# Performance work log

Measured on AMD Instinct MI355X. Metric: run time of the kernel, lower is better.

The kernel has to match this reference:

```python
import jax, jax.numpy as jnp
import numpy as np

N, E, D, H, C, G, L = 100000, 1600000, 128, 4, 32, 4096, 3  # nodes, edges, h_dim, heads, head_dim, graphs, conv blocks


def setup_inputs() -> dict:
    key = jax.random.key(0)
    ks = jax.random.split(key, 24)
    s = 0.05
    w = lambda k, shape: jax.random.normal(k, shape, jnp.float32) * s
    inp = {
        "x": jax.random.normal(ks[0], (N, D), jnp.float32),
        "edge_index": jax.random.randint(ks[1], (2, E), 0, N),
        "batch": jnp.sort(jax.random.randint(ks[2], (N,), 0, G)),
        # input TransformerConv (in=D, out=C per head, H heads, beta=True)
        "in_Wq": w(ks[3], (D, D)), "in_bq": jnp.zeros((D,), jnp.float32),
        "in_Wk": w(ks[4], (D, D)), "in_bk": jnp.zeros((D,), jnp.float32),
        "in_Wv": w(ks[5], (D, D)), "in_bv": jnp.zeros((D,), jnp.float32),
        "in_Ws": w(ks[6], (D, D)), "in_bs": jnp.zeros((D,), jnp.float32),
        "in_Wbeta": w(ks[7], (3 * D,)),
        # stacked conv blocks (L of them, in=out=D)
        "blk_Wq": w(ks[8], (L, D, D)), "blk_bq": jnp.zeros((L, D), jnp.float32),
        "blk_Wk": w(ks[9], (L, D, D)), "blk_bk": jnp.zeros((L, D), jnp.float32),
        "blk_Wv": w(ks[10], (L, D, D)), "blk_bv": jnp.zeros((L, D), jnp.float32),
        "blk_Ws": w(ks[11], (L, D, D)), "blk_bs": jnp.zeros((L, D), jnp.float32),
        "blk_Wbeta": w(ks[12], (L, 3 * D)),
        # MLP head
        "W1": w(ks[13], (D, 64)), "b1": jnp.zeros((64,), jnp.float32),
        "W2": w(ks[14], (64, 32)), "b2": jnp.zeros((32,), jnp.float32),
        "W3": w(ks[15], (32, 1)), "b3": jnp.zeros((1,), jnp.float32),
    }
    return inp


def transformer_conv(x, src, dst, Wq, bq, Wk, bk, Wv, bv, Ws, bs, Wbeta):
    # PyG TransformerConv, concat=True, root_weight=True, beta=True, eval mode
    q = (x @ Wq + bq).reshape(N, H, C)
    k = (x @ Wk + bk).reshape(N, H, C)
    v = (x @ Wv + bv).reshape(N, H, C)
    # per-edge attention logits: message j=src -> i=dst
    alpha = jnp.einsum("ehc,ehc->eh", q[dst], k[src]) / jnp.sqrt(jnp.float32(C))  # [E,H]
    m = jax.ops.segment_max(alpha, dst, num_segments=N)
    m = jnp.where(jnp.isfinite(m), m, 0.0)
    e = jnp.exp(alpha - m[dst])
    denom = jax.ops.segment_sum(e, dst, num_segments=N)
    a = e / (denom[dst] + 1e-16)  # segment softmax over in-edges of dst
    msg = a[..., None] * v[src]  # [E,H,C]
    out = jax.ops.segment_sum(msg, dst, num_segments=N).reshape(N, H * C)
    x_r = x @ Ws + bs
    beta = jax.nn.sigmoid(jnp.concatenate([out, x_r, out - x_r], axis=-1) @ Wbeta)[:, None]
    return beta * x_r + (1.0 - beta) * out


def reference(x, edge_index, batch, in_Wq, in_bq, in_Wk, in_bk, in_Wv, in_bv,
              in_Ws, in_bs, in_Wbeta, blk_Wq, blk_bq, blk_Wk, blk_bk, blk_Wv,
              blk_bv, blk_Ws, blk_bs, blk_Wbeta, W1, b1, W2, b2, W3, b3):
    src, dst = edge_index[0], edge_index[1]
    h = jax.nn.relu(transformer_conv(x, src, dst, in_Wq, in_bq, in_Wk, in_bk,
                                     in_Wv, in_bv, in_Ws, in_bs, in_Wbeta))
    for l in range(L):  # dropout is identity in eval mode
        h = jax.nn.relu(transformer_conv(h, src, dst, blk_Wq[l], blk_bq[l],
                                         blk_Wk[l], blk_bk[l], blk_Wv[l], blk_bv[l],
                                         blk_Ws[l], blk_bs[l], blk_Wbeta[l]))
    # global mean pool over graphs
    sums = jax.ops.segment_sum(h, batch, num_segments=G)
    cnt = jax.ops.segment_sum(jnp.ones((N, 1), h.dtype), batch, num_segments=G)
    g = sums / jnp.maximum(cnt, 1.0)
    g = jax.nn.relu(g @ W1 + b1)
    g = jax.nn.relu(g @ W2 + b2)
    return jax.nn.sigmoid(g @ W3 + b3)
```

## Files before the change

### kernel.cpp

```cpp
#include <hip/hip_runtime.h>
#include <hip/hip_bf16.h>
#include <cstdint>

#define DH 128
#define NB 256
#define NBK 1024

typedef __attribute__((ext_vector_type(8))) short short8;
typedef __attribute__((ext_vector_type(4))) float floatx4;
typedef __attribute__((ext_vector_type(2))) float floatx2;

__device__ __forceinline__ float bflo(unsigned u) { return __uint_as_float(u << 16); }
__device__ __forceinline__ float bfhi(unsigned u) { return __uint_as_float(u & 0xffff0000u); }

__device__ __forceinline__ unsigned pk_bf16(float a, float b) {
  return ((unsigned)__bfloat16_as_ushort(__float2bfloat16(b)) << 16)
       | (unsigned)__bfloat16_as_ushort(__float2bfloat16(a));
}

template<int CTRL>
__device__ __forceinline__ float dpp_add(float x) {
  int y = __builtin_amdgcn_update_dpp(0, __float_as_int(x), CTRL, 0xf, 0xf, true);
  return x + __int_as_float(y);
}


__global__ __launch_bounds__(256)
void csr_p1(const int* __restrict__ dst, int* __restrict__ hist, int E, int chunk) {
  __shared__ int cnt[NBK];
  const int blk = blockIdx.x, tid = threadIdx.x;
  for (int c = tid; c < NBK; c += 256) cnt[c] = 0;
  __syncthreads();
  int base = blk * chunk;
  int end = base + chunk; if (end > E) end = E;
  for (int e = base + tid; e < end; e += 256) atomicAdd(&cnt[dst[e] >> 7], 1);
  __syncthreads();
  for (int c = tid; c < NBK; c += 256) hist[c * NB + blk] = cnt[c];
}

__global__ __launch_bounds__(256)
void csr_p2(int* __restrict__ hist, int* __restrict__ total) {
  int b = blockIdx.x * 4 + (threadIdx.x >> 6);
  int lane = threadIdx.x & 63;
  int4 v = *(int4*)&hist[b * NB + lane * 4];
  int s0 = v.x;
  int s1 = s0 + v.y;
  int s2 = s1 + v.z;
  int s3 = s2 + v.w;
  int t = s3;
  for (int d = 1; d < 64; d <<= 1) {
    int y = __shfl_up(t, d);
    if (lane >= d) t += y;
  }
  int excl = t - s3;
  int4 o;
  o.x = excl; o.y = excl + s0; o.z = excl + s1; o.w = excl + s2;
  *(int4*)&hist[b * NB + lane * 4] = o;
  if (lane == 63) total[b] = t;
}

__global__ __launch_bounds__(1024)
void scan_tstart(const int* __restrict__ total, int* __restrict__ tstart) {
  __shared__ int sh[1024];
  int t = threadIdx.x;
  int v = total[t];
  sh[t] = v;
  __syncthreads();
  for (int d = 1; d < 1024; d <<= 1) {
    int x = (t >= d) ? sh[t - d] : 0;
    __syncthreads();
    sh[t] += x;
    __syncthreads();
  }
  tstart[t] = sh[t] - v;
}

__global__ __launch_bounds__(256)
void csr_p3(const int* __restrict__ src, const int* __restrict__ dst,
            const int* __restrict__ hist, const int* __restrict__ tstart,
            int* __restrict__ part, int E, int chunk) {
  __shared__ int cur[NBK];
  const int blk = blockIdx.x, tid = threadIdx.x;
  for (int c = tid; c < NBK; c += 256) cur[c] = hist[c * NB + blk] + tstart[c];
  __syncthreads();
  int base = blk * chunk;
  int end = base + chunk; if (end > E) end = E;
  for (int e = base + tid; e < end; e += 256) {
    int d = dst[e];
    int b = d >> 7;
    int pos = atomicAdd(&cur[b], 1);
    part[pos] = (src[e] << 7) | (d & 127);
  }
}

__global__ __launch_bounds__(256)
void csr_p4(const int* __restrict__ part, const int* __restrict__ tstart,
            const int* __restrict__ total, int* __restrict__ deg,
            int* __restrict__ off, int* __restrict__ csr, int Nn) {
  __shared__ int lcnt[128], lscan[128], lcur[128];
  const int b = blockIdx.x, tid = threadIdx.x;
  const int p0 = tstart[b];
  const int m = total[b];
  if (tid < 128) lcnt[tid] = 0;
  __syncthreads();
  for (int k = tid; k < m; k += 256) atomicAdd(&lcnt[part[p0 + k] & 127], 1);
  __syncthreads();
  if (tid < 128) lscan[tid] = lcnt[tid];
  __syncthreads();
  for (int d = 1; d < 128; d <<= 1) {
    int v = 0;
    if (tid < 128 && tid >= d) v = lscan[tid - d];
    __syncthreads();
    if (tid < 128) lscan[tid] += v;
    __syncthreads();
  }
  if (tid < 128) {
    int ex = lscan[tid] - lcnt[tid];
    lcur[tid] = ex;
    int n = (b << 7) + tid;
    if (n < Nn) { deg[n] = lcnt[tid]; off[n] = p0 + ex; }
  }
  __syncthreads();
  for (int k = tid; k < m; k += 256) {
    int pk = part[p0 + k];
    int pos = p0 + atomicAdd(&lcur[pk & 127], 1);
    csr[pos] = pk >> 7;
  }
}


__global__ void goff_kernel(const int* __restrict__ batch, int* __restrict__ goff,
                            int N, int G) {
  int g = blockIdx.x * 256 + threadIdx.x;
  if (g > G) return;
  if (g == G) { goff[G] = N; return; }
  int lo = 0, hi = N;
  while (lo < hi) { int mid = (lo + hi) >> 1; if (batch[mid] < g) lo = mid + 1; else hi = mid; }
  goff[g] = lo;
}


__global__ __launch_bounds__(256)
void pack_w_kernel(const float* __restrict__ iWq, const float* __restrict__ iWk,
                   const float* __restrict__ iWv, const float* __restrict__ iWs,
                   const float* __restrict__ ibq, const float* __restrict__ ibk,
                   const float* __restrict__ ibv, const float* __restrict__ ibs,
                   const float* __restrict__ bWq, const float* __restrict__ bWk,
                   const float* __restrict__ bWv, const float* __restrict__ bWs,
                   const float* __restrict__ bbq, const float* __restrict__ bbk,
                   const float* __restrict__ bbv, const float* __restrict__ bbs,
                   __hip_bfloat16* __restrict__ WT2, float* __restrict__ bcat) {
  const int layer = blockIdx.x / 65;
  const int bid = blockIdx.x % 65;
  const float *Wq, *Wk, *Wv, *Ws, *bq, *bk, *bv, *bs;
  if (layer == 0) {
    Wq = iWq; Wk = iWk; Wv = iWv; Ws = iWs; bq = ibq; bk = ibk; bv = ibv; bs = ibs;
  } else {
    int m = layer - 1;
    Wq = bWq + (size_t)m * DH * DH; Wk = bWk + (size_t)m * DH * DH;
    Wv = bWv + (size_t)m * DH * DH; Ws = bWs + (size_t)m * DH * DH;
    bq = bbq + (size_t)m * DH; bk = bbk + (size_t)m * DH;
    bv = bbv + (size_t)m * DH; bs = bbs + (size_t)m * DH;
  }
  unsigned short* WT2l = (unsigned short*)WT2 + (size_t)layer * 65536;
  float* bcl = bcat + layer * 512;

  if (bid == 64) {
    for (int c = threadIdx.x; c < 512; c += 256) {
      int which = c >> 7, cc = c & 127;
      const float* b = (which == 0) ? bq : (which == 1) ? bk : (which == 2) ? bv : bs;
      bcl[c] = b[cc];
    }
    return;
  }
  __shared__ float tile[32][33];
  const int which = bid >> 4, kb = (bid >> 2) & 3, cb = bid & 3;
  const float* W = (which == 0) ? Wq : (which == 1) ? Wk : (which == 2) ? Wv : Ws;
  const int tx = threadIdx.x & 31, ty = threadIdx.x >> 5;
#pragma unroll
  for (int r = ty; r < 32; r += 8)
    tile[r][tx] = W[(kb * 32 + r) * 128 + cb * 32 + tx];
  __syncthreads();
  const int t = threadIdx.x;
  const int mt_sel = t >> 7;
  const int s4 = (t & 127) * 4;
  const int l16 = s4 >> 5;
  const int quad = (s4 >> 3) & 3;
  const int j0 = s4 & 7;
  const int cl = mt_sel * 16 + l16;
  const int kr = quad * 8 + j0;
  float f0 = tile[kr + 0][cl];
  float f1 = tile[kr + 1][cl];
  float f2 = tile[kr + 2][cl];
  float f3 = tile[kr + 3][cl];
  const int mt = which * 8 + cb * 2 + mt_sel;
  const int o = mt * 2048 + kb * 512 + l16 * 32 + quad * 8 + j0;
  uint2 w;
  w.x = pk_bf16(f0, f1);
  w.y = pk_bf16(f2, f3);
  *(uint2*)&WT2l[o] = w;
}


template<int F32IN>
__global__ __launch_bounds__(256)
void gemm_qkvs(const void* __restrict__ Xin, const short* __restrict__ WT2,
               const float* __restrict__ bc,
               unsigned int* __restrict__ qout,
               unsigned int* __restrict__ kvp,
               unsigned int* __restrict__ xrout, int Nn) {
  __shared__ short As[32][132];
  const int row0 = blockIdx.x * 32;
  const int tid = threadIdx.x;

#pragma unroll
  for (int p = 0; p < 2; ++p) {
    int chunk = p * 256 + tid;
    int r = chunk >> 4, c8 = chunk & 15;
    int row = row0 + r; if (row >= Nn) row = Nn - 1;
    if (F32IN) {
      const float* xf = (const float*)Xin + (size_t)row * 128 + c8 * 8;
      float4 f0 = *(const float4*)xf;
      float4 f1 = *(const float4*)(xf + 4);
      int4 pk;
      ((unsigned*)&pk)[0] = pk_bf16(f0.x, f0.y);
      ((unsigned*)&pk)[1] = pk_bf16(f0.z, f0.w);
      ((unsigned*)&pk)[2] = pk_bf16(f1.x, f1.y);
      ((unsigned*)&pk)[3] = pk_bf16(f1.z, f1.w);
      *(int4*)&As[r][c8 * 8] = pk;
    } else {
      *(int4*)&As[r][c8 * 8] = *(const int4*)((const short*)Xin + (size_t)row * 128 + c8 * 8);
    }
  }
  __syncthreads();

  const int w = tid >> 6, lane = tid & 63, quad = lane >> 4, l16 = lane & 15;

  short8 xf[2][4];
#pragma unroll
  for (int nt = 0; nt < 2; ++nt)
#pragma unroll
    for (int kt = 0; kt < 4; ++kt)
      xf[nt][kt] = *(const short8*)&As[nt * 16 + l16][kt * 32 + quad * 8];

  const int fbase = l16 * 32 + quad * 8;

  if (w == 0 || w == 3) {
    unsigned int* outp = (w == 0) ? qout : xrout;
    const int mbase = (w == 0) ? 0 : 24;
#pragma unroll
    for (int i = 0; i < 8; ++i) {
      const int mt = mbase + i;
      short8 af[4];
#pragma unroll
      for (int kt = 0; kt < 4; ++kt)
        af[kt] = *(const short8*)&WT2[mt * 2048 + kt * 512 + fbase];
      float4 bias = *(const float4*)&bc[mt * 16 + quad * 4];
      const int wc = (i * 16 + quad * 4);
#pragma unroll
      for (int nt = 0; nt < 2; ++nt) {
        floatx4 acc = (floatx4){0.f, 0.f, 0.f, 0.f};
#pragma unroll
        for (int kt = 0; kt < 4; ++kt)
          acc = __builtin_amdgcn_mfma_f32_16x16x32_bf16(af[kt], xf[nt][kt], acc, 0, 0, 0);
        int node = row0 + nt * 16 + l16;
        if (node < Nn) {
          uint2 o;
          o.x = pk_bf16(acc[0] + bias.x, acc[1] + bias.y);
          o.y = pk_bf16(acc[2] + bias.z, acc[3] + bias.w);
          *(uint2*)&outp[(size_t)node * 64 + (wc >> 1)] = o;
        }
      }
    }
  } else {
    const int kb = 8 + (w - 1) * 4;
    const int vb = 16 + (w - 1) * 4;
#pragma unroll
    for (int i = 0; i < 4; ++i) {
      const int mk = kb + i, mv = vb + i;
      short8 afk[4], afv[4];
#pragma unroll
      for (int kt = 0; kt < 4; ++kt) {
        afk[kt] = *(const short8*)&WT2[mk * 2048 + kt * 512 + fbase];
        afv[kt] = *(const short8*)&WT2[mv * 2048 + kt * 512 + fbase];
      }
      float4 bk4 = *(const float4*)&bc[mk * 16 + quad * 4];
      float4 bv4 = *(const float4*)&bc[mv * 16 + quad * 4];
      const int krel = (w - 1) * 64 + i * 16 + quad * 4;
#pragma unroll
      for (int nt = 0; nt < 2; ++nt) {
        floatx4 ak = (floatx4){0.f, 0.f, 0.f, 0.f};
        floatx4 av = (floatx4){0.f, 0.f, 0.f, 0.f};
#pragma unroll
        for (int kt = 0; kt < 4; ++kt) {
          ak = __builtin_amdgcn_mfma_f32_16x16x32_bf16(afk[kt], xf[nt][kt], ak, 0, 0, 0);
          av = __builtin_amdgcn_mfma_f32_16x16x32_bf16(afv[kt], xf[nt][kt], av, 0, 0, 0);
        }
        int node = row0 + nt * 16 + l16;
        if (node < Nn) {
          int d0 = __builtin_amdgcn_cvt_pk_fp8_f32(ak[0] + bk4.x, ak[1] + bk4.y, 0, false);
          d0 = __builtin_amdgcn_cvt_pk_fp8_f32(av[0] + bv4.x, av[1] + bv4.y, d0, true);
          int d1 = __builtin_amdgcn_cvt_pk_fp8_f32(ak[2] + bk4.z, ak[3] + bk4.w, 0, false);
          d1 = __builtin_amdgcn_cvt_pk_fp8_f32(av[2] + bv4.z, av[3] + bv4.w, d1, true);
          uint2 o; o.x = (unsigned)d0; o.y = (unsigned)d1;
          *(uint2*)&kvp[(size_t)node * 64 + (krel >> 1)] = o;
        }
      }
    }
  }
}


__global__ __launch_bounds__(128)
void attn_kernel(unsigned int* __restrict__ q_h, const uint4* __restrict__ kvq,
                 const uint4* __restrict__ xr4, const int* __restrict__ off,
                 const int* __restrict__ deg, const int* __restrict__ csr,
                 const float* __restrict__ Wb, int Nn) {
  int wv = __builtin_amdgcn_readfirstlane(threadIdx.x >> 6);
  int i = blockIdx.x * 2 + wv;
  if (i >= Nn) return;
  const int l = threadIdx.x & 63;
  const int j = l & 15;
  const int g = l >> 4;

  const float QS = 0.17677669529663687f * 1.4426950408889634f;
  uint4 qw = ((const uint4*)q_h)[(size_t)i * 16 + j];
  float q0 = bflo(qw.x) * QS, q1 = bfhi(qw.x) * QS;
  float q2 = bflo(qw.y) * QS, q3 = bfhi(qw.y) * QS;
  float q4 = bflo(qw.z) * QS, q5 = bfhi(qw.z) * QS;
  float q6 = bflo(qw.w) * QS, q7 = bfhi(qw.w) * QS;

  const int e0 = off[i];
  const int dg = deg[i];
  const int eend = e0 + dg;

  float denA = 0.f, denB = 0.f;
  float aA[8] = {0.f, 0.f, 0.f, 0.f, 0.f, 0.f, 0.f, 0.f};
  float aB[8] = {0.f, 0.f, 0.f, 0.f, 0.f, 0.f, 0.f, 0.f};

  auto comp = [&](const uint4& kv, bool valid, float& den, float (&a)[8]) {
    floatx2 k0 = __builtin_amdgcn_cvt_pk_f32_fp8((int)kv.x, false);
    floatx2 v0 = __builtin_amdgcn_cvt_pk_f32_fp8((int)kv.x, true);
    floatx2 k1 = __builtin_amdgcn_cvt_pk_f32_fp8((int)kv.y, false);
    floatx2 v1 = __builtin_amdgcn_cvt_pk_f32_fp8((int)kv.y, true);
    floatx2 k2 = __builtin_amdgcn_cvt_pk_f32_fp8((int)kv.z, false);
    floatx2 v2 = __builtin_amdgcn_cvt_pk_f32_fp8((int)kv.z, true);
    floatx2 k3 = __builtin_amdgcn_cvt_pk_f32_fp8((int)kv.w, false);
    floatx2 v3 = __builtin_amdgcn_cvt_pk_f32_fp8((int)kv.w, true);
    float d = q0 * k0.x + q1 * k0.y + q2 * k1.x + q3 * k1.y
            + q4 * k2.x + q5 * k2.y + q6 * k3.x + q7 * k3.y;
    d = dpp_add<0xB1>(d);
    d = dpp_add<0x4E>(d);
    float p = valid ? exp2f(d) : 0.f;
    den += p;
    a[0] += p * v0.x; a[1] += p * v0.y; a[2] += p * v1.x; a[3] += p * v1.y;
    a[4] += p * v2.x; a[5] += p * v2.y; a[6] += p * v3.x; a[7] += p * v3.y;
  };

  for (int e = e0; e < eend; e += 64) {
    const int rem = eend - e;
    const int take = (rem < 64) ? rem : 64;
    int il = e + l; if (il >= eend) il = eend - 1;
    const int sv = csr[il];

    for (int base = 0; base < take; base += 32) {
      const int left = take - base;
      const int ns = (left + 3) >> 2 < 8 ? (left + 3) >> 2 : 8;
      int sarr[8];
      bool pv[8];
#pragma unroll
      for (int u = 0; u < 8; ++u) {
        if (u < ns) {
          int c = base + u * 4 + g;
          pv[u] = c < take;
          sarr[u] = __shfl(sv, pv[u] ? c : 0);
        }
      }
      uint4 kv[8];
#pragma unroll
      for (int u = 0; u < 8; ++u)
        if (u < ns) kv[u] = kvq[(unsigned)((sarr[u] << 4) | j)];
#pragma unroll
      for (int u = 0; u < 8; ++u)
        if (u < ns) comp(kv[u], pv[u], (u & 1) ? denB : denA, (u & 1) ? aB : aA);
    }
  }

  uint4 xw = xr4[(size_t)i * 16 + j];
  float4 wo0 = *(const float4*)&Wb[8 * j];
  float4 wo1 = *(const float4*)&Wb[8 * j + 4];
  float4 wx0 = *(const float4*)&Wb[128 + 8 * j];
  float4 wx1 = *(const float4*)&Wb[128 + 8 * j + 4];
  float4 wd0 = *(const float4*)&Wb[256 + 8 * j];
  float4 wd1 = *(const float4*)&Wb[256 + 8 * j + 4];

  float den = denA + denB;
  float a0 = aA[0] + aB[0], a1 = aA[1] + aB[1], a2 = aA[2] + aB[2], a3 = aA[3] + aB[3];
  float a4 = aA[4] + aB[4], a5 = aA[5] + aB[5], a6 = aA[6] + aB[6], a7 = aA[7] + aB[7];

  den += __shfl_xor(den, 16); den += __shfl_xor(den, 32);
  a0 += __shfl_xor(a0, 16); a0 += __shfl_xor(a0, 32);
  a1 += __shfl_xor(a1, 16); a1 += __shfl_xor(a1, 32);
  a2 += __shfl_xor(a2, 16); a2 += __shfl_xor(a2, 32);
  a3 += __shfl_xor(a3, 16); a3 += __shfl_xor(a3, 32);
  a4 += __shfl_xor(a4, 16); a4 += __shfl_xor(a4, 32);
  a5 += __shfl_xor(a5, 16); a5 += __shfl_xor(a5, 32);
  a6 += __shfl_xor(a6, 16); a6 += __shfl_xor(a6, 32);
  a7 += __shfl_xor(a7, 16); a7 += __shfl_xor(a7, 32);

  float inv = 1.f / (den + 1e-16f);
  float o0 = a0 * inv, o1 = a1 * inv, o2 = a2 * inv, o3 = a3 * inv;
  float o4 = a4 * inv, o5 = a5 * inv, o6 = a6 * inv, o7 = a7 * inv;

  float x0 = bflo(xw.x), x1 = bfhi(xw.x);
  float x2 = bflo(xw.y), x3 = bfhi(xw.y);
  float x4 = bflo(xw.z), x5 = bfhi(xw.z);
  float x6 = bflo(xw.w), x7 = bfhi(xw.w);

  float c = o0 * wo0.x + o1 * wo0.y + o2 * wo0.z + o3 * wo0.w
          + o4 * wo1.x + o5 * wo1.y + o6 * wo1.z + o7 * wo1.w
          + x0 * wx0.x + x1 * wx0.y + x2 * wx0.z + x3 * wx0.w
          + x4 * wx1.x + x5 * wx1.y + x6 * wx1.z + x7 * wx1.w
          + (o0 - x0) * wd0.x + (o1 - x1) * wd0.y + (o2 - x2) * wd0.z + (o3 - x3) * wd0.w
          + (o4 - x4) * wd1.x + (o5 - x5) * wd1.y + (o6 - x6) * wd1.z + (o7 - x7) * wd1.w;
  c = dpp_add<0xB1>(c);
  c = dpp_add<0x4E>(c);
  c = dpp_add<0x141>(c);
  c = dpp_add<0x140>(c);
  float beta = 1.f / (1.f + __expf(-c));

  if (g == 0) {
    float h0 = fmaxf(beta * x0 + (1.f - beta) * o0, 0.f);
    float h1 = fmaxf(beta * x1 + (1.f - beta) * o1, 0.f);
    float h2 = fmaxf(beta * x2 + (1.f - beta) * o2, 0.f);
    float h3 = fmaxf(beta * x3 + (1.f - beta) * o3, 0.f);
    float h4 = fmaxf(beta * x4 + (1.f - beta) * o4, 0.f);
    float h5 = fmaxf(beta * x5 + (1.f - beta) * o5, 0.f);
    float h6 = fmaxf(beta * x6 + (1.f - beta) * o6, 0.f);
    float h7 = fmaxf(beta * x7 + (1.f - beta) * o7, 0.f);
    uint4 hw;
    hw.x = pk_bf16(h0, h1);
    hw.y = pk_bf16(h2, h3);
    hw.z = pk_bf16(h4, h5);
    hw.w = pk_bf16(h6, h7);
    ((uint4*)q_h)[(size_t)i * 16 + j] = hw;
  }
}


__global__ __launch_bounds__(128)
void poolmlp_kernel(const unsigned short* __restrict__ h, const int* __restrict__ goff,
                    const float* __restrict__ W1, const float* __restrict__ b1,
                    const float* __restrict__ W2, const float* __restrict__ b2,
                    const float* __restrict__ W3, const float* __restrict__ b3,
                    float* __restrict__ out) {
  int g = blockIdx.x;
  int t = threadIdx.x;
  int n0 = goff[g], cnt = goff[g + 1] - n0;
  float s = 0.f;
  for (int n = n0; n < n0 + cnt; ++n) s += bflo(h[(size_t)n * 128 + t]);
  __shared__ float gv[128];
  __shared__ float t1[64];
  __shared__ float t2[32];
  gv[t] = s / fmaxf((float)cnt, 1.0f);
  __syncthreads();
  if (t < 64) {
    float a = b1[t];
    for (int k = 0; k < 128; ++k) a += gv[k] * W1[k * 64 + t];
    t1[t] = fmaxf(a, 0.f);
  }
  __syncthreads();
  if (t < 32) {
    float a = b2[t];
    for (int k = 0; k < 64; ++k) a += t1[k] * W2[k * 32 + t];
    t2[t] = fmaxf(a, 0.f);
  }
  __syncthreads();
  if (t == 0) {
    float a = b3[0];
    for (int k = 0; k < 32; ++k) a += t2[k] * W3[k];
    out[g] = 1.f / (1.f + __expf(-a));
  }
}


extern "C" void kernel_launch(void* const* d_in, const int* in_sizes, int n_in,
                              void* d_out, int out_size, void* d_ws, size_t ws_size,
                              hipStream_t stream) {
  const float* x = (const float*)d_in[0];
  const int* edge_index = (const int*)d_in[1];
  const int* batch = (const int*)d_in[2];
  const int N = in_sizes[0] / DH;
  const int E = in_sizes[1] / 2;
  const int G = out_size;
  const int* src = edge_index;
  const int* dst = edge_index + E;

  const float* in_Wq = (const float*)d_in[3];
  const float* in_bq = (const float*)d_in[4];
  const float* in_Wk = (const float*)d_in[5];
  const float* in_bk = (const float*)d_in[6];
  const float* in_Wv = (const float*)d_in[7];
  const float* in_bv = (const float*)d_in[8];
  const float* in_Ws = (const float*)d_in[9];
  const float* in_bs = (const float*)d_in[10];
  const float* in_Wbeta = (const float*)d_in[11];
  const float* blk_Wq = (const float*)d_in[12];
  const float* blk_bq = (const float*)d_in[13];
  const float* blk_Wk = (const float*)d_in[14];
  const float* blk_bk = (const float*)d_in[15];
  const float* blk_Wv = (const float*)d_in[16];
  const float* blk_bv = (const float*)d_in[17];
  const float* blk_Ws = (const float*)d_in[18];
  const float* blk_bs = (const float*)d_in[19];
  const float* blk_Wbeta = (const float*)d_in[20];

  char* p = (char*)d_ws;
  auto take = [&](size_t bytes) { char* r = p; p += (bytes + 255) & ~(size_t)255; return r; };
  __hip_bfloat16* h0 = (__hip_bfloat16*)take((size_t)N * DH * 2);
  __hip_bfloat16* h1 = (__hip_bfloat16*)take((size_t)N * DH * 2);
  unsigned char* kvp = (unsigned char*)take((size_t)N * 256);
  unsigned short* xr = (unsigned short*)take((size_t)N * DH * 2);
  __hip_bfloat16* WT2 = (__hip_bfloat16*)take((size_t)4 * 512 * DH * 2);
  float* bcat = (float*)take((size_t)4 * 512 * 4);
  int* deg    = (int*)take((size_t)N * 4);
  int* off    = (int*)take((size_t)N * 4);
  int* csr    = (int*)take((size_t)E * 4);
  int* part   = (int*)take((size_t)E * 4);
  int* hist   = (int*)take((size_t)NB * NBK * 4);
  int* total  = (int*)take(NBK * 4);
  int* tstart = (int*)take(NBK * 4);
  int* goff   = (int*)take((size_t)(G + 1) * 4);
  (void)n_in;
  if ((size_t)(p - (char*)d_ws) > ws_size) return;

  const int NBUCK = (N + 127) >> 7;
  const int chunk = (E + NB - 1) / NB;

  csr_p1<<<NB, 256, 0, stream>>>(dst, hist, E, chunk);
  csr_p2<<<NBK / 4, 256, 0, stream>>>(hist, total);
  scan_tstart<<<1, 1024, 0, stream>>>(total, tstart);
  csr_p3<<<NB, 256, 0, stream>>>(src, dst, hist, tstart, part, E, chunk);
  csr_p4<<<NBUCK, 256, 0, stream>>>(part, tstart, total, deg, off, csr, N);

  goff_kernel<<<(G + 256) / 256, 256, 0, stream>>>(batch, goff, N, G);

  pack_w_kernel<<<4 * 65, 256, 0, stream>>>(
      in_Wq, in_Wk, in_Wv, in_Ws, in_bq, in_bk, in_bv, in_bs,
      blk_Wq, blk_Wk, blk_Wv, blk_Ws, blk_bq, blk_bk, blk_bv, blk_bs,
      WT2, bcat);

  for (int l = 0; l < 4; ++l) {
    const float* Wb = (l == 0) ? in_Wbeta : blk_Wbeta + (size_t)(l - 1) * 3 * DH;
    const short* WT2l = (const short*)WT2 + (size_t)l * 65536;
    const float* bcl = bcat + (size_t)l * 512;
    __hip_bfloat16* hin  = (l & 1) ? h1 : h0;
    __hip_bfloat16* qbuf = (l & 1) ? h0 : h1;
    if (l == 0) {
      gemm_qkvs<1><<<(N + 31) / 32, 256, 0, stream>>>((const void*)x, WT2l, bcl,
          (unsigned int*)qbuf, (unsigned int*)kvp, (unsigned int*)xr, N);
    } else {
      gemm_qkvs<0><<<(N + 31) / 32, 256, 0, stream>>>((const void*)hin, WT2l, bcl,
          (unsigned int*)qbuf, (unsigned int*)kvp, (unsigned int*)xr, N);
    }
    attn_kernel<<<(N + 1) / 2, 128, 0, stream>>>((unsigned int*)qbuf, (const uint4*)kvp,
        (const uint4*)xr, off, deg, csr, Wb, N);
  }

  poolmlp_kernel<<<G, 128, 0, stream>>>((const unsigned short*)h0, goff,
      (const float*)d_in[21], (const float*)d_in[22],
      (const float*)d_in[23], (const float*)d_in[24],
      (const float*)d_in[25], (const float*)d_in[26],
      (float*)d_out);
}
```

Measured before the change: 788.6 us.

## Process two destination nodes per wavefront in attention and pack offset/degree

The attention kernel now handles two destination nodes per 64-lane wavefront. Their gathered K/V loads are interleaved so more memory requests are in flight per wave, and the block grows to 4 waves (8 nodes). CSR offset and degree are merged into a single int2 array, so one load fetches both. In exchange, registers per thread roughly double (two q vectors and two accumulators), which may lower occupancy, and a wave's loop now runs for the larger of the two nodes' degrees.

```diff
diff --git a/kernel.cpp b/kernel.cpp
--- a/kernel.cpp
+++ b/kernel.cpp
@@ -95,8 +95,8 @@
 
 __global__ __launch_bounds__(256)
 void csr_p4(const int* __restrict__ part, const int* __restrict__ tstart,
-            const int* __restrict__ total, int* __restrict__ deg,
-            int* __restrict__ off, int* __restrict__ csr, int Nn) {
+            const int* __restrict__ total, int2* __restrict__ offdeg,
+            int* __restrict__ csr, int Nn) {
   __shared__ int lcnt[128], lscan[128], lcur[128];
   const int b = blockIdx.x, tid = threadIdx.x;
   const int p0 = tstart[b];
@@ -118,7 +118,7 @@
     int ex = lscan[tid] - lcnt[tid];
     lcur[tid] = ex;
     int n = (b << 7) + tid;
-    if (n < Nn) { deg[n] = lcnt[tid]; off[n] = p0 + ex; }
+    if (n < Nn) offdeg[n] = make_int2(p0 + ex, lcnt[tid]);
   }
   __syncthreads();
   for (int k = tid; k < m; k += 256) {
@@ -311,34 +311,41 @@
 }
 
 
-__global__ __launch_bounds__(128)
+__global__ __launch_bounds__(256)
 void attn_kernel(unsigned int* __restrict__ q_h, const uint4* __restrict__ kvq,
-                 const uint4* __restrict__ xr4, const int* __restrict__ off,
-                 const int* __restrict__ deg, const int* __restrict__ csr,
-                 const float* __restrict__ Wb, int Nn) {
+                 const uint4* __restrict__ xr4, const int2* __restrict__ offdeg,
+                 const int* __restrict__ csr, const float* __restrict__ Wb, int Nn) {
   int wv = __builtin_amdgcn_readfirstlane(threadIdx.x >> 6);
-  int i = blockIdx.x * 2 + wv;
-  if (i >= Nn) return;
+  int iA = blockIdx.x * 8 + wv * 2;
+  if (iA >= Nn) return;
+  const int iB = iA + 1;
+  const bool hasB = iB < Nn;
   const int l = threadIdx.x & 63;
   const int j = l & 15;
   const int g = l >> 4;
 
   const float QS = 0.17677669529663687f * 1.4426950408889634f;
-  uint4 qw = ((const uint4*)q_h)[(size_t)i * 16 + j];
-  float q0 = bflo(qw.x) * QS, q1 = bfhi(qw.x) * QS;
-  float q2 = bflo(qw.y) * QS, q3 = bfhi(qw.y) * QS;
-  float q4 = bflo(qw.z) * QS, q5 = bfhi(qw.z) * QS;
-  float q6 = bflo(qw.w) * QS, q7 = bfhi(qw.w) * QS;
-
-  const int e0 = off[i];
-  const int dg = deg[i];
-  const int eend = e0 + dg;
+  const uint4* qh4 = (const uint4*)q_h;
+  uint4 qwA = qh4[(size_t)iA * 16 + j];
+  uint4 qwB = hasB ? qh4[(size_t)iB * 16 + j] : qwA;
+  int2 odA = offdeg[iA];
+  int2 odB = hasB ? offdeg[iB] : make_int2(0, 0);
+
+  float qA[8], qB[8];
+  qA[0] = bflo(qwA.x) * QS; qA[1] = bfhi(qwA.x) * QS;
+  qA[2] = bflo(qwA.y) * QS; qA[3] = bfhi(qwA.y) * QS;
+  qA[4] = bflo(qwA.z) * QS; qA[5] = bfhi(qwA.z) * QS;
+  qA[6] = bflo(qwA.w) * QS; qA[7] = bfhi(qwA.w) * QS;
+  qB[0] = bflo(qwB.x) * QS; qB[1] = bfhi(qwB.x) * QS;
+  qB[2] = bflo(qwB.y) * QS; qB[3] = bfhi(qwB.y) * QS;
+  qB[4] = bflo(qwB.z) * QS; qB[5] = bfhi(qwB.z) * QS;
+  qB[6] = bflo(qwB.w) * QS; qB[7] = bfhi(qwB.w) * QS;
 
   float denA = 0.f, denB = 0.f;
-  float aA[8] = {0.f, 0.f, 0.f, 0.f, 0.f, 0.f, 0.f, 0.f};
-  float aB[8] = {0.f, 0.f, 0.f, 0.f, 0.f, 0.f, 0.f, 0.f};
-
-  auto comp = [&](const uint4& kv, bool valid, float& den, float (&a)[8]) {
+  float accA[8] = {0.f, 0.f, 0.f, 0.f, 0.f, 0.f, 0.f, 0.f};
+  float accB[8] = {0.f, 0.f, 0.f, 0.f, 0.f, 0.f, 0.f, 0.f};
+
+  auto comp = [&](const uint4& kv, bool valid, const float (&q)[8], float& den, float (&a)[8]) {
     floatx2 k0 = __builtin_amdgcn_cvt_pk_f32_fp8((int)kv.x, false);
     floatx2 v0 = __builtin_amdgcn_cvt_pk_f32_fp8((int)kv.x, true);
     floatx2 k1 = __builtin_amdgcn_cvt_pk_f32_fp8((int)kv.y, false);
@@ -347,8 +354,8 @@
     floatx2 v2 = __builtin_amdgcn_cvt_pk_f32_fp8((int)kv.z, true);
     floatx2 k3 = __builtin_amdgcn_cvt_pk_f32_fp8((int)kv.w, false);
     floatx2 v3 = __builtin_amdgcn_cvt_pk_f32_fp8((int)kv.w, true);
-    float d = q0 * k0.x + q1 * k0.y + q2 * k1.x + q3 * k1.y
-            + q4 * k2.x + q5 * k2.y + q6 * k3.x + q7 * k3.y;
+    float d = q[0] * k0.x + q[1] * k0.y + q[2] * k1.x + q[3] * k1.y
+            + q[4] * k2.x + q[5] * k2.y + q[6] * k3.x + q[7] * k3.y;
     d = dpp_add<0xB1>(d);
     d = dpp_add<0x4E>(d);
     float p = valid ? exp2f(d) : 0.f;
@@ -357,36 +364,45 @@
     a[4] += p * v2.x; a[5] += p * v2.y; a[6] += p * v3.x; a[7] += p * v3.y;
   };
 
-  for (int e = e0; e < eend; e += 64) {
-    const int rem = eend - e;
-    const int take = (rem < 64) ? rem : 64;
-    int il = e + l; if (il >= eend) il = eend - 1;
-    const int sv = csr[il];
-
-    for (int base = 0; base < take; base += 32) {
-      const int left = take - base;
-      const int ns = (left + 3) >> 2 < 8 ? (left + 3) >> 2 : 8;
-      int sarr[8];
-      bool pv[8];
-#pragma unroll
-      for (int u = 0; u < 8; ++u) {
-        if (u < ns) {
-          int c = base + u * 4 + g;
-          pv[u] = c < take;
-          sarr[u] = __shfl(sv, pv[u] ? c : 0);
-        }
+  int eA = odA.x, remA = odA.y;
+  int eB = odB.x, remB = odB.y;
+  while (remA > 0 || remB > 0) {
+    const int takeA = (remA < 64) ? remA : 64;
+    const int takeB = (remB < 64) ? remB : 64;
+    int svA = 0, svB = 0;
+    if (takeA > 0) { int il = (l < takeA) ? l : takeA - 1; svA = csr[eA + il]; }
+    if (takeB > 0) { int il = (l < takeB) ? l : takeB - 1; svB = csr[eB + il]; }
+    const int mx = (takeA > takeB) ? takeA : takeB;
+
+    for (int b = 0; b < mx; b += 16) {
+      uint4 kvA[4], kvB[4];
+      bool pA[4], pB[4], fA[4], fB[4];
+#pragma unroll
+      for (int u = 0; u < 4; ++u) {
+        int c = b + u * 4 + g;
+        fA[u] = (b + u * 4) < takeA;
+        pA[u] = c < takeA;
+        if (fA[u]) { int s = __shfl(svA, pA[u] ? c : 0); kvA[u] = kvq[(unsigned)((s << 4) | j)]; }
       }
-      uint4 kv[8];
-#pragma unroll
-      for (int u = 0; u < 8; ++u)
-        if (u < ns) kv[u] = kvq[(unsigned)((sarr[u] << 4) | j)];
-#pragma unroll
-      for (int u = 0; u < 8; ++u)
-        if (u < ns) comp(kv[u], pv[u], (u & 1) ? denB : denA, (u & 1) ? aB : aA);
-    }
-  }
-
-  uint4 xw = xr4[(size_t)i * 16 + j];
+#pragma unroll
+      for (int u = 0; u < 4; ++u) {
+        int c = b + u * 4 + g;
+        fB[u] = (b + u * 4) < takeB;
+        pB[u] = c < takeB;
+        if (fB[u]) { int s = __shfl(svB, pB[u] ? c : 0); kvB[u] = kvq[(unsigned)((s << 4) | j)]; }
+      }
+#pragma unroll
+      for (int u = 0; u < 4; ++u) {
+        if (fA[u]) comp(kvA[u], pA[u], qA, denA, accA);
+        if (fB[u]) comp(kvB[u], pB[u], qB, denB, accB);
+      }
+    }
+    remA -= takeA; eA += takeA;
+    remB -= takeB; eB += takeB;
+  }
+
+  uint4 xwA = xr4[(size_t)iA * 16 + j];
+  uint4 xwB = hasB ? xr4[(size_t)iB * 16 + j] : xwA;
   float4 wo0 = *(const float4*)&Wb[8 * j];
   float4 wo1 = *(const float4*)&Wb[8 * j + 4];
   float4 wx0 = *(const float4*)&Wb[128 + 8 * j];
@@ -394,57 +410,52 @@
   float4 wd0 = *(const float4*)&Wb[256 + 8 * j];
   float4 wd1 = *(const float4*)&Wb[256 + 8 * j + 4];
 
-  float den = denA + denB;
-  float a0 = aA[0] + aB[0], a1 = aA[1] + aB[1], a2 = aA[2] + aB[2], a3 = aA[3] + aB[3];
-  float a4 = aA[4] + aB[4], a5 = aA[5] + aB[5], a6 = aA[6] + aB[6], a7 = aA[7] + aB[7];
-
-  den += __shfl_xor(den, 16); den += __shfl_xor(den, 32);
-  a0 += __shfl_xor(a0, 16); a0 += __shfl_xor(a0, 32);
-  a1 += __shfl_xor(a1, 16); a1 += __shfl_xor(a1, 32);
-  a2 += __shfl_xor(a2, 16); a2 += __shfl_xor(a2, 32);
-  a3 += __shfl_xor(a3, 16); a3 += __shfl_xor(a3, 32);
-  a4 += __shfl_xor(a4, 16); a4 += __shfl_xor(a4, 32);
-  a5 += __shfl_xor(a5, 16); a5 += __shfl_xor(a5, 32);
-  a6 += __shfl_xor(a6, 16); a6 += __shfl_xor(a6, 32);
-  a7 += __shfl_xor(a7, 16); a7 += __shfl_xor(a7, 32);
-
-  float inv = 1.f / (den + 1e-16f);
-  float o0 = a0 * inv, o1 = a1 * inv, o2 = a2 * inv, o3 = a3 * inv;
-  float o4 = a4 * inv, o5 = a5 * inv, o6 = a6 * inv, o7 = a7 * inv;
-
-  float x0 = bflo(xw.x), x1 = bfhi(xw.x);
-  float x2 = bflo(xw.y), x3 = bfhi(xw.y);
-  float x4 = bflo(xw.z), x5 = bfhi(xw.z);
-  float x6 = bflo(xw.w), x7 = bfhi(xw.w);
-
-  float c = o0 * wo0.x + o1 * wo0.y + o2 * wo0.z + o3 * wo0.w
-          + o4 * wo1.x + o5 * wo1.y + o6 * wo1.z + o7 * wo1.w
-          + x0 * wx0.x + x1 * wx0.y + x2 * wx0.z + x3 * wx0.w
-          + x4 * wx1.x + x5 * wx1.y + x6 * wx1.z + x7 * wx1.w
-          + (o0 - x0) * wd0.x + (o1 - x1) * wd0.y + (o2 - x2) * wd0.z + (o3 - x3) * wd0.w
-          + (o4 - x4) * wd1.x + (o5 - x5) * wd1.y + (o6 - x6) * wd1.z + (o7 - x7) * wd1.w;
-  c = dpp_add<0xB1>(c);
-  c = dpp_add<0x4E>(c);
-  c = dpp_add<0x141>(c);
-  c = dpp_add<0x140>(c);
-  float beta = 1.f / (1.f + __expf(-c));
-
-  if (g == 0) {
-    float h0 = fmaxf(beta * x0 + (1.f - beta) * o0, 0.f);
-    float h1 = fmaxf(beta * x1 + (1.f - beta) * o1, 0.f);
-    float h2 = fmaxf(beta * x2 + (1.f - beta) * o2, 0.f);
-    float h3 = fmaxf(beta * x3 + (1.f - beta) * o3, 0.f);
-    float h4 = fmaxf(beta * x4 + (1.f - beta) * o4, 0.f);
-    float h5 = fmaxf(beta * x5 + (1.f - beta) * o5, 0.f);
-    float h6 = fmaxf(beta * x6 + (1.f - beta) * o6, 0.f);
-    float h7 = fmaxf(beta * x7 + (1.f - beta) * o7, 0.f);
-    uint4 hw;
-    hw.x = pk_bf16(h0, h1);
-    hw.y = pk_bf16(h2, h3);
-    hw.z = pk_bf16(h4, h5);
-    hw.w = pk_bf16(h6, h7);
-    ((uint4*)q_h)[(size_t)i * 16 + j] = hw;
-  }
+  denA += __shfl_xor(denA, 16); denA += __shfl_xor(denA, 32);
+  denB += __shfl_xor(denB, 16); denB += __shfl_xor(denB, 32);
+#pragma unroll
+  for (int d = 0; d < 8; ++d) {
+    accA[d] += __shfl_xor(accA[d], 16); accA[d] += __shfl_xor(accA[d], 32);
+    accB[d] += __shfl_xor(accB[d], 16); accB[d] += __shfl_xor(accB[d], 32);
+  }
+
+  auto epi = [&](float den, const float (&a)[8], const uint4& xw, int node, int gsel) {
+    float inv = 1.f / (den + 1e-16f);
+    float o0 = a[0] * inv, o1 = a[1] * inv, o2 = a[2] * inv, o3 = a[3] * inv;
+    float o4 = a[4] * inv, o5 = a[5] * inv, o6 = a[6] * inv, o7 = a[7] * inv;
+    float x0 = bflo(xw.x), x1 = bfhi(xw.x);
+    float x2 = bflo(xw.y), x3 = bfhi(xw.y);
+    float x4 = bflo(xw.z), x5 = bfhi(xw.z);
+    float x6 = bflo(xw.w), x7 = bfhi(xw.w);
+    float c = o0 * wo0.x + o1 * wo0.y + o2 * wo0.z + o3 * wo0.w
+            + o4 * wo1.x + o5 * wo1.y + o6 * wo1.z + o7 * wo1.w
+            + x0 * wx0.x + x1 * wx0.y + x2 * wx0.z + x3 * wx0.w
+            + x4 * wx1.x + x5 * wx1.y + x6 * wx1.z + x7 * wx1.w
+            + (o0 - x0) * wd0.x + (o1 - x1) * wd0.y + (o2 - x2) * wd0.z + (o3 - x3) * wd0.w
+            + (o4 - x4) * wd1.x + (o5 - x5) * wd1.y + (o6 - x6) * wd1.z + (o7 - x7) * wd1.w;
+    c = dpp_add<0xB1>(c);
+    c = dpp_add<0x4E>(c);
+    c = dpp_add<0x141>(c);
+    c = dpp_add<0x140>(c);
+    float beta = 1.f / (1.f + __expf(-c));
+    if (g == gsel) {
+      float h0 = fmaxf(beta * x0 + (1.f - beta) * o0, 0.f);
+      float h1 = fmaxf(beta * x1 + (1.f - beta) * o1, 0.f);
+      float h2 = fmaxf(beta * x2 + (1.f - beta) * o2, 0.f);
+      float h3 = fmaxf(beta * x3 + (1.f - beta) * o3, 0.f);
+      float h4 = fmaxf(beta * x4 + (1.f - beta) * o4, 0.f);
+      float h5 = fmaxf(beta * x5 + (1.f - beta) * o5, 0.f);
+      float h6 = fmaxf(beta * x6 + (1.f - beta) * o6, 0.f);
+      float h7 = fmaxf(beta * x7 + (1.f - beta) * o7, 0.f);
+      uint4 hw;
+      hw.x = pk_bf16(h0, h1);
+      hw.y = pk_bf16(h2, h3);
+      hw.z = pk_bf16(h4, h5);
+      hw.w = pk_bf16(h6, h7);
+      ((uint4*)q_h)[(size_t)node * 16 + j] = hw;
+    }
+  };
+  epi(denA, accA, xwA, iA, 0);
+  if (hasB) epi(denB, accB, xwB, iB, 1);
 }
 
 
@@ -523,8 +534,7 @@
   unsigned short* xr = (unsigned short*)take((size_t)N * DH * 2);
   __hip_bfloat16* WT2 = (__hip_bfloat16*)take((size_t)4 * 512 * DH * 2);
   float* bcat = (float*)take((size_t)4 * 512 * 4);
-  int* deg    = (int*)take((size_t)N * 4);
-  int* off    = (int*)take((size_t)N * 4);
+  int2* offdeg = (int2*)take((size_t)N * 8);
   int* csr    = (int*)take((size_t)E * 4);
   int* part   = (int*)take((size_t)E * 4);
   int* hist   = (int*)take((size_t)NB * NBK * 4);
@@ -541,7 +551,7 @@
   csr_p2<<<NBK / 4, 256, 0, stream>>>(hist, total);
   scan_tstart<<<1, 1024, 0, stream>>>(total, tstart);
   csr_p3<<<NB, 256, 0, stream>>>(src, dst, hist, tstart, part, E, chunk);
-  csr_p4<<<NBUCK, 256, 0, stream>>>(part, tstart, total, deg, off, csr, N);
+  csr_p4<<<NBUCK, 256, 0, stream>>>(part, tstart, total, offdeg, csr, N);
 
   goff_kernel<<<(G + 256) / 256, 256, 0, stream>>>(batch, goff, N, G);
 
@@ -563,8 +573,8 @@
       gemm_qkvs<0><<<(N + 31) / 32, 256, 0, stream>>>((const void*)hin, WT2l, bcl,
           (unsigned int*)qbuf, (unsigned int*)kvp, (unsigned int*)xr, N);
     }
-    attn_kernel<<<(N + 1) / 2, 128, 0, stream>>>((unsigned int*)qbuf, (const uint4*)kvp,
-        (const uint4*)xr, off, deg, csr, Wb, N);
+    attn_kernel<<<(N + 7) / 8, 256, 0, stream>>>((unsigned int*)qbuf, (const uint4*)kvp,
+        (const uint4*)xr, offdeg, csr, Wb, N);
   }
 
   poolmlp_kernel<<<G, 128, 0, stream>>>((const unsigned short*)h0, goff,
```

After: 750.8 us. 4.8% less time.
